# Optimization experiments

Measured on AMD Instinct MI355X. Metric: run time of the kernel, lower is better.

## Reference

```python
import jax, jax.numpy as jnp
import numpy as np

N_SRC0, N_DST0 = 100000, 20000   # block0: 100k src -> 20k dst
N_DST1 = 4096                    # block1: 20k src -> 4096 dst (seed nodes)


def setup_inputs() -> dict:
    key = jax.random.key(0)
    ks = jax.random.split(key, 8)
    E0, E1 = 640000, 131072
    return {
        "features": jax.random.normal(ks[0], (N_SRC0, 256), jnp.float32),
        "W1": jax.random.normal(ks[1], (256, 256), jnp.float32) * (1.0 / np.sqrt(256)),
        "b1": jnp.zeros((256,), jnp.float32),
        "W2": jax.random.normal(ks[2], (256, 128), jnp.float32) * (1.0 / np.sqrt(256)),
        "b2": jnp.zeros((128,), jnp.float32),
        "src0": jax.random.randint(ks[3], (E0,), 0, N_SRC0, jnp.int32),
        "dst0": jax.random.randint(ks[4], (E0,), 0, N_DST0, jnp.int32),
        "src1": jax.random.randint(ks[5], (E1,), 0, N_DST0, jnp.int32),
        "dst1": jax.random.randint(ks[6], (E1,), 0, N_DST1, jnp.int32),
    }


def _graph_conv(src, dst, n_dst, feat, W, b):
    # DGL GraphConv, norm='both': D_out^{-1/2} gather-sum D_in^{-1/2}, then WX+b.
    n_src = feat.shape[0]
    ones = jnp.ones(src.shape[0], feat.dtype)
    out_deg = jax.ops.segment_sum(ones, src, num_segments=n_src)
    norm_src = jnp.clip(out_deg, 1.0, None) ** -0.5          # [n_src]
    h = feat * norm_src[:, None]
    agg = jax.ops.segment_sum(h[src], dst, num_segments=n_dst)  # sparse SpMM
    in_deg = jax.ops.segment_sum(ones, dst, num_segments=n_dst)
    norm_dst = jnp.clip(in_deg, 1.0, None) ** -0.5           # [n_dst]
    return (agg * norm_dst[:, None]) @ W + b


def reference(features, W1, b1, W2, b2, src0, dst0, src1, dst1):
    x = jax.nn.relu(_graph_conv(src0, dst0, N_DST0, features, W1, b1))
    x = _graph_conv(src1, dst1, N_DST1, x, W2, b2)
    return x
```

## Files before the change

### kernel.cpp

```cpp
#include <hip/hip_runtime.h>
#include <hip/hip_bf16.h>

#define K_DIM 256
#define RSTRIDE 128

#define EPB   8192
#define G0_DB 625
#define G0_SB 256
#define G0_SW 392
#define G1_DB 128
#define G1_SB 64
#define G1_SW 313
#define BCAP  2048
#define SCAP  4096
#define GPAD  16

typedef short bf16x8 __attribute__((ext_vector_type(8)));
typedef float f32x4 __attribute__((ext_vector_type(4)));

static __device__ __forceinline__ unsigned short f2bf(float x) {
    __hip_bfloat16 b = __float2bfloat16(x);
    return *reinterpret_cast<unsigned short*>(&b);
}
static __device__ __forceinline__ float bflo(unsigned int p) {
    return __uint_as_float(p << 16);
}
static __device__ __forceinline__ float bfhi(unsigned int p) {
    return __uint_as_float(p & 0xffff0000u);
}

template <int NDB, int NSB, int SW>
static __device__ __forceinline__ void split_graph(
        const int* __restrict__ src, const int* __restrict__ dst, int E, int chunk,
        int* __restrict__ gdc, int* __restrict__ gsc,
        unsigned int* __restrict__ bdst, unsigned int* __restrict__ bsrc,
        int* sh) {
    int* histD = sh;
    int* histS = sh + NDB;
    int* baseD = sh + NDB + NSB;
    int* baseS = baseD + NDB;
    const int tid = threadIdx.x;
    const int e0 = chunk * EPB;
    const int n = min(EPB, E - e0);
    for (int i = tid; i < NDB + NSB; i += 256) sh[i] = 0;
    __syncthreads();
    for (int j = tid; j < n; j += 256) {
        int d = dst[e0 + j];
        int s = src[e0 + j];
        atomicAdd(&histD[d >> 5], 1);
        atomicAdd(&histS[(int)((unsigned)s / SW)], 1);
    }
    __syncthreads();
    for (int i = tid; i < NDB; i += 256) {
        int h = histD[i];
        baseD[i] = h ? atomicAdd(&gdc[i * GPAD], h) : 0;
        histD[i] = 0;
    }
    for (int i = tid; i < NSB; i += 256) {
        int h = histS[i];
        baseS[i] = h ? atomicAdd(&gsc[i * GPAD], h) : 0;
        histS[i] = 0;
    }
    __syncthreads();
    for (int j = tid; j < n; j += 256) {
        int d = dst[e0 + j];
        int s = src[e0 + j];
        int bD = d >> 5;
        int rD = atomicAdd(&histD[bD], 1) + baseD[bD];
        if (rD < BCAP) bdst[(size_t)bD * BCAP + rD] = ((unsigned)s << 5) | (unsigned)(d & 31);
        int bS = (int)((unsigned)s / SW);
        int rS = atomicAdd(&histS[bS], 1) + baseS[bS];
        if (rS < SCAP) bsrc[(size_t)bS * SCAP + rS] = (unsigned)s;
    }
}

__global__ __launch_bounds__(256) void split_mega_kernel(
        const int* __restrict__ src0, const int* __restrict__ dst0, int E0,
        const int* __restrict__ src1, const int* __restrict__ dst1, int E1,
        int* __restrict__ gdc0, int* __restrict__ gsc0,
        unsigned int* __restrict__ bdst0, unsigned int* __restrict__ bsrc0,
        int* __restrict__ gdc1, int* __restrict__ gsc1,
        unsigned int* __restrict__ bdst1, unsigned int* __restrict__ bsrc1,
        int nA0, int nA1,
        const float* __restrict__ feat, unsigned short* __restrict__ h, int total_f,
        int castBlocks,
        const float* __restrict__ W1, uint4* __restrict__ pw1,
        const float* __restrict__ W2, uint4* __restrict__ pw2) {
    __shared__ int sh[2 * (G0_DB + G0_SB)];
    const int b = blockIdx.x;
    if (b < nA0) {
        split_graph<G0_DB, G0_SB, G0_SW>(src0, dst0, E0, b, gdc0, gsc0, bdst0, bsrc0, sh);
    } else if (b < nA0 + nA1) {
        split_graph<G1_DB, G1_SB, G1_SW>(src1, dst1, E1, b - nA0, gdc1, gsc1, bdst1, bsrc1, sh);
    } else if (b < nA0 + nA1 + castBlocks) {
        int idx = ((b - nA0 - nA1) * blockDim.x + threadIdx.x) * 8;
        if (idx >= total_f) return;
        const float4 v0 = *reinterpret_cast<const float4*>(feat + idx);
        const float4 v1 = *reinterpret_cast<const float4*>(feat + idx + 4);
        union { ushort4 u4[2]; uint4 u; } o;
        o.u4[0].x = f2bf(v0.x); o.u4[0].y = f2bf(v0.y);
        o.u4[0].z = f2bf(v0.z); o.u4[0].w = f2bf(v0.w);
        o.u4[1].x = f2bf(v1.x); o.u4[1].y = f2bf(v1.y);
        o.u4[1].z = f2bf(v1.z); o.u4[1].w = f2bf(v1.w);
        *reinterpret_cast<uint4*>(h + idx) = o.u;
    } else if (b < nA0 + nA1 + castBlocks + 32) {
        int idx = (b - nA0 - nA1 - castBlocks) * blockDim.x + threadIdx.x;
        int lane = idx & 63;
        int kt = (idx >> 6) & 7;
        int nt = idx >> 9;
        int n = nt * 16 + (lane & 15);
        int k = kt * 32 + (lane >> 4) * 8;
        union { unsigned short us[8]; uint4 u; } o;
#pragma unroll
        for (int j = 0; j < 8; ++j) o.us[j] = f2bf(W1[(size_t)(k + j) * 256 + n]);
        pw1[idx] = o.u;
    } else {
        int idx = (b - nA0 - nA1 - castBlocks - 32) * blockDim.x + threadIdx.x;
        int lane = idx & 63;
        int kt = (idx >> 6) & 7;
        int nt = idx >> 9;
        int n = nt * 16 + (lane & 15);
        int k = kt * 32 + (lane >> 4) * 8;
        union { unsigned short us[8]; uint4 u; } o;
#pragma unroll
        for (int j = 0; j < 8; ++j) o.us[j] = f2bf(W2[(size_t)(k + j) * 128 + n]);
        pw2[idx] = o.u;
    }
}

__global__ __launch_bounds__(256) void finalize_kernel(
        const unsigned int* __restrict__ bdst0, const int* __restrict__ gdc0,
        int* __restrict__ cnt0, int* __restrict__ esrc0,
        const unsigned int* __restrict__ bdst1, const int* __restrict__ gdc1,
        int* __restrict__ cnt1, int* __restrict__ esrc1,
        const unsigned int* __restrict__ bsrc0, const int* __restrict__ gsc0,
        int* __restrict__ od0,
        const unsigned int* __restrict__ bsrc1, const int* __restrict__ gsc1,
        int* __restrict__ od1) {
    __shared__ int sh[G0_SW];
    const int tid = threadIdx.x;
    int b = blockIdx.x;
    if (b < G0_DB + G1_DB) {
        const bool g0 = b < G0_DB;
        if (!g0) b -= G0_DB;
        const unsigned int* __restrict__ bd = g0 ? bdst0 : bdst1;
        const int nb = min((g0 ? gdc0 : gdc1)[b * GPAD], BCAP);
        int* __restrict__ esrc = g0 ? esrc0 : esrc1;
        int* __restrict__ cnt = g0 ? cnt0 : cnt1;
        if (tid < 32) sh[tid] = 0;
        __syncthreads();
        for (int j = tid; j < nb; j += 256) {
            unsigned v = bd[(size_t)b * BCAP + j];
            int dloc = v & 31;
            int s = v >> 5;
            int slot = atomicAdd(&sh[dloc], 1);
            if (slot < RSTRIDE) esrc[((size_t)(b * 32 + dloc) << 7) + slot] = s;
        }
        __syncthreads();
        if (tid < 32) cnt[b * 32 + tid] = sh[tid];
    } else {
        b -= G0_DB + G1_DB;
        const bool g0 = b < G0_SB;
        if (!g0) b -= G0_SB;
        const unsigned int* __restrict__ bs = g0 ? bsrc0 : bsrc1;
        const int SW = g0 ? G0_SW : G1_SW;
        const int NN = g0 ? 100000 : 20000;
        const int nb = min((g0 ? gsc0 : gsc1)[b * GPAD], SCAP);
        int* __restrict__ od = g0 ? od0 : od1;
        for (int i = tid; i < SW; i += 256) sh[i] = 0;
        __syncthreads();
        const int base = b * SW;
        for (int j = tid; j < nb; j += 256) {
            int v = (int)bs[(size_t)b * SCAP + j];
            atomicAdd(&sh[v - base], 1);
        }
        __syncthreads();
        for (int i = tid; i < SW; i += 256) {
            int node = base + i;
            if (node < NN) od[node] = sh[i];
        }
    }
}

template <bool NORM>
__global__ __launch_bounds__(256) void gather_bf16_kernel(
        const unsigned short* __restrict__ hfeat, const int* __restrict__ esrc,
        const int* __restrict__ cnt, const int* __restrict__ od,
        unsigned short* __restrict__ aggb, int n_dst) {
    int row = blockIdx.x * (blockDim.x >> 6) + (threadIdx.x >> 6);
    int lane = threadIdx.x & 63;
    if (row >= n_dst) return;
    const int c = cnt[row];
    const int cend = min(c, RSTRIDE);
    const int* __restrict__ ep = esrc + ((size_t)row << 7);
    float a0 = 0.f, a1 = 0.f, a2 = 0.f, a3 = 0.f;
    int i = 0;
    for (; i + 3 < cend; i += 4) {
        int s0 = ep[i];
        int s1 = ep[i + 1];
        int s2 = ep[i + 2];
        int s3 = ep[i + 3];
        float n0 = NORM ? rsqrtf((float)max(od[s0], 1)) : 1.0f;
        float n1 = NORM ? rsqrtf((float)max(od[s1], 1)) : 1.0f;
        float n2 = NORM ? rsqrtf((float)max(od[s2], 1)) : 1.0f;
        float n3 = NORM ? rsqrtf((float)max(od[s3], 1)) : 1.0f;
        const uint2 p0 = *reinterpret_cast<const uint2*>(hfeat + (((size_t)s0) << 8) + lane * 4);
        const uint2 p1 = *reinterpret_cast<const uint2*>(hfeat + (((size_t)s1) << 8) + lane * 4);
        const uint2 p2 = *reinterpret_cast<const uint2*>(hfeat + (((size_t)s2) << 8) + lane * 4);
        const uint2 p3 = *reinterpret_cast<const uint2*>(hfeat + (((size_t)s3) << 8) + lane * 4);
        if (NORM) {
            a0 = fmaf(bflo(p0.x), n0, a0); a1 = fmaf(bfhi(p0.x), n0, a1);
            a2 = fmaf(bflo(p0.y), n0, a2); a3 = fmaf(bfhi(p0.y), n0, a3);
            a0 = fmaf(bflo(p1.x), n1, a0); a1 = fmaf(bfhi(p1.x), n1, a1);
            a2 = fmaf(bflo(p1.y), n1, a2); a3 = fmaf(bfhi(p1.y), n1, a3);
            a0 = fmaf(bflo(p2.x), n2, a0); a1 = fmaf(bfhi(p2.x), n2, a1);
            a2 = fmaf(bflo(p2.y), n2, a2); a3 = fmaf(bfhi(p2.y), n2, a3);
            a0 = fmaf(bflo(p3.x), n3, a0); a1 = fmaf(bfhi(p3.x), n3, a1);
            a2 = fmaf(bflo(p3.y), n3, a2); a3 = fmaf(bfhi(p3.y), n3, a3);
        } else {
            a0 += (bflo(p0.x) + bflo(p1.x)) + (bflo(p2.x) + bflo(p3.x));
            a1 += (bfhi(p0.x) + bfhi(p1.x)) + (bfhi(p2.x) + bfhi(p3.x));
            a2 += (bflo(p0.y) + bflo(p1.y)) + (bflo(p2.y) + bflo(p3.y));
            a3 += (bfhi(p0.y) + bfhi(p1.y)) + (bfhi(p2.y) + bfhi(p3.y));
        }
    }
    for (; i < cend; ++i) {
        int s0 = ep[i];
        float n0 = NORM ? rsqrtf((float)max(od[s0], 1)) : 1.0f;
        const uint2 p0 = *reinterpret_cast<const uint2*>(hfeat + (((size_t)s0) << 8) + lane * 4);
        if (NORM) {
            a0 = fmaf(bflo(p0.x), n0, a0); a1 = fmaf(bfhi(p0.x), n0, a1);
            a2 = fmaf(bflo(p0.y), n0, a2); a3 = fmaf(bfhi(p0.y), n0, a3);
        } else {
            a0 += bflo(p0.x);
            a1 += bfhi(p0.x);
            a2 += bflo(p0.y);
            a3 += bfhi(p0.y);
        }
    }
    float nd = rsqrtf((float)max(c, 1));
    ushort4 o;
    o.x = f2bf(a0 * nd);
    o.y = f2bf(a1 * nd);
    o.z = f2bf(a2 * nd);
    o.w = f2bf(a3 * nd);
    *reinterpret_cast<ushort4*>(aggb + (((size_t)row) << 8) + lane * 4) = o;
}

__global__ __launch_bounds__(256) void gemm0_mfma_kernel(
        const unsigned short* __restrict__ hA, const uint4* __restrict__ pW,
        const float* __restrict__ bias, const int* __restrict__ od1,
        unsigned short* __restrict__ out, int M) {
    const int m0 = blockIdx.x * 16;
    const int w = threadIdx.x >> 6;
    const int lane = threadIdx.x & 63;

    bf16x8 a[8];
    const unsigned short* ap = hA + (size_t)(m0 + (lane & 15)) * K_DIM + (lane >> 4) * 8;
#pragma unroll
    for (int kt = 0; kt < 8; ++kt)
        a[kt] = *reinterpret_cast<const bf16x8*>(ap + kt * 32);

    const int rbase = m0 + (lane >> 4) * 4;
    float nsv[4];
#pragma unroll
    for (int r = 0; r < 4; ++r) nsv[r] = rsqrtf((float)max(od1[rbase + r], 1));

#pragma unroll
    for (int nt = 0; nt < 4; ++nt) {
        const int n0 = w * 64 + nt * 16;
        f32x4 acc = {0.f, 0.f, 0.f, 0.f};
#pragma unroll
        for (int kt = 0; kt < 8; ++kt) {
            bf16x8 b = *reinterpret_cast<const bf16x8*>(&pW[((size_t)(n0 >> 4) * 8 + kt) * 64 + lane]);
            acc = __builtin_amdgcn_mfma_f32_16x16x32_bf16(a[kt], b, acc, 0, 0, 0);
        }
        const int col = n0 + (lane & 15);
        const float bv = bias[col];
#pragma unroll
        for (int r = 0; r < 4; ++r) {
            float v = fmaxf(acc[r] + bv, 0.0f) * nsv[r];
            out[(size_t)(rbase + r) * K_DIM + col] = f2bf(v);
        }
    }
}

__global__ __launch_bounds__(256) void gemm1_mfma_kernel(
        const unsigned short* __restrict__ hA, const uint4* __restrict__ pW,
        const float* __restrict__ bias, float* __restrict__ out, int M) {
    const int m0 = blockIdx.x * 16;
    const int w = threadIdx.x >> 6;
    const int lane = threadIdx.x & 63;

    bf16x8 a[8];
    const unsigned short* ap = hA + (size_t)(m0 + (lane & 15)) * K_DIM + (lane >> 4) * 8;
#pragma unroll
    for (int kt = 0; kt < 8; ++kt)
        a[kt] = *reinterpret_cast<const bf16x8*>(ap + kt * 32);

    const int rbase = m0 + (lane >> 4) * 4;
#pragma unroll
    for (int nt = 0; nt < 2; ++nt) {
        const int n0 = w * 32 + nt * 16;
        f32x4 acc = {0.f, 0.f, 0.f, 0.f};
#pragma unroll
        for (int kt = 0; kt < 8; ++kt) {
            bf16x8 b = *reinterpret_cast<const bf16x8*>(&pW[((size_t)(n0 >> 4) * 8 + kt) * 64 + lane]);
            acc = __builtin_amdgcn_mfma_f32_16x16x32_bf16(a[kt], b, acc, 0, 0, 0);
        }
        const int col = n0 + (lane & 15);
        const float bv = bias[col];
#pragma unroll
        for (int r = 0; r < 4; ++r)
            out[(size_t)(rbase + r) * 128 + col] = acc[r] + bv;
    }
}

__global__ __launch_bounds__(256) void gatherf_kernel(
        const float* __restrict__ feat, const int* __restrict__ esrc,
        const int* __restrict__ cnt, const int* __restrict__ od,
        float* __restrict__ outbuf, int n_dst) {
    int row = blockIdx.x * (blockDim.x >> 6) + (threadIdx.x >> 6);
    int lane = threadIdx.x & 63;
    if (row >= n_dst) return;
    const int c = cnt[row];
    const int cend = min(c, RSTRIDE);
    const int* __restrict__ ep = esrc + ((size_t)row << 7);
    float4 acc = {0.f, 0.f, 0.f, 0.f};
    for (int i = 0; i < cend; ++i) {
        int s0 = ep[i];
        float n0 = rsqrtf((float)max(od[s0], 1));
        const float4 v0 = *reinterpret_cast<const float4*>(feat + (((size_t)s0) << 8) + lane * 4);
        acc.x = fmaf(v0.x, n0, acc.x); acc.y = fmaf(v0.y, n0, acc.y);
        acc.z = fmaf(v0.z, n0, acc.z); acc.w = fmaf(v0.w, n0, acc.w);
    }
    float nd = rsqrtf((float)max(c, 1));
    float4 o = {acc.x * nd, acc.y * nd, acc.z * nd, acc.w * nd};
    *reinterpret_cast<float4*>(outbuf + (((size_t)row) << 8) + lane * 4) = o;
}

__global__ void edges_kernel(const int* __restrict__ src0, const int* __restrict__ dst0,
                             int* __restrict__ od0, int* __restrict__ cnt0,
                             int* __restrict__ esrc0, int E0,
                             const int* __restrict__ src1, const int* __restrict__ dst1,
                             int* __restrict__ od1, int* __restrict__ cnt1,
                             int* __restrict__ esrc1, int E1) {
    int i = blockIdx.x * blockDim.x + threadIdx.x;
    if (i < E0) {
        int s = src0[i];
        int d = dst0[i];
        atomicAdd(&od0[s], 1);
        int slot = atomicAdd(&cnt0[d], 1);
        if (slot < RSTRIDE) esrc0[(d << 7) + slot] = s;
    } else if (i < E0 + E1) {
        int e = i - E0;
        int s = src1[e];
        int d = dst1[e];
        atomicAdd(&od1[s], 1);
        int slot = atomicAdd(&cnt1[d], 1);
        if (slot < RSTRIDE) esrc1[(d << 7) + slot] = s;
    }
}

template <int ROWS, int NCOLS, bool RELU>
__global__ __launch_bounds__(NCOLS) void gemm_kernel(
        const float* __restrict__ A, const float* __restrict__ W,
        const float* __restrict__ bias, float* __restrict__ out, int M) {
    const int row0 = blockIdx.x * ROWS;
    const int c = threadIdx.x;
    const float* __restrict__ Ablk = A + (size_t)row0 * K_DIM;
    const float* __restrict__ Wc = W + c;

    float acc[ROWS];
#pragma unroll
    for (int r = 0; r < ROWS; ++r) acc[r] = 0.0f;

    float w0 = Wc[0];
    float w1 = Wc[NCOLS];
    float w2 = Wc[2 * NCOLS];
    float w3 = Wc[3 * NCOLS];

#pragma unroll 2
    for (int k = 0; k < K_DIM - 4; k += 4) {
        const float* p = Wc + (size_t)(k + 4) * NCOLS;
        float n0 = p[0];
        float n1 = p[NCOLS];
        float n2 = p[2 * NCOLS];
        float n3 = p[3 * NCOLS];
#pragma unroll
        for (int r = 0; r < ROWS; ++r) {
            const float4 a = *reinterpret_cast<const float4*>(Ablk + r * K_DIM + k);
            acc[r] = fmaf(a.x, w0, acc[r]);
            acc[r] = fmaf(a.y, w1, acc[r]);
            acc[r] = fmaf(a.z, w2, acc[r]);
            acc[r] = fmaf(a.w, w3, acc[r]);
        }
        w0 = n0; w1 = n1; w2 = n2; w3 = n3;
    }
    {
        const int k = K_DIM - 4;
#pragma unroll
        for (int r = 0; r < ROWS; ++r) {
            const float4 a = *reinterpret_cast<const float4*>(Ablk + r * K_DIM + k);
            acc[r] = fmaf(a.x, w0, acc[r]);
            acc[r] = fmaf(a.y, w1, acc[r]);
            acc[r] = fmaf(a.z, w2, acc[r]);
            acc[r] = fmaf(a.w, w3, acc[r]);
        }
    }

    const float b = bias[c];
#pragma unroll
    for (int r = 0; r < ROWS; ++r) {
        float v = acc[r] + b;
        if (RELU) v = fmaxf(v, 0.0f);
        out[(size_t)(row0 + r) * NCOLS + c] = v;
    }
}

extern "C" void kernel_launch(void* const* d_in, const int* in_sizes, int n_in,
                              void* d_out, int out_size, void* d_ws, size_t ws_size,
                              hipStream_t stream) {
    const float* features = (const float*)d_in[0];
    const float* W1 = (const float*)d_in[1];
    const float* b1 = (const float*)d_in[2];
    const float* W2 = (const float*)d_in[3];
    const float* b2 = (const float*)d_in[4];
    const int* src0 = (const int*)d_in[5];
    const int* dst0 = (const int*)d_in[6];
    const int* src1 = (const int*)d_in[7];
    const int* dst1 = (const int*)d_in[8];
    const int E0 = in_sizes[5];
    const int E1 = in_sizes[7];
    const int NSRC0 = 100000, NDST0 = 20000, NDST1 = 4096;

    char* ws = (char*)d_ws;
    size_t off = 0;
    auto carve = [&](size_t bytes) -> void* {
        void* p = ws + off;
        off = (off + bytes + 255) & ~(size_t)255;
        return p;
    };
    int* gdc0 = (int*)carve((size_t)G0_DB * GPAD * 4);
    int* gsc0 = (int*)carve((size_t)G0_SB * GPAD * 4);
    int* gdc1 = (int*)carve((size_t)G1_DB * GPAD * 4);
    int* gsc1 = (int*)carve((size_t)G1_SB * GPAD * 4);
    const size_t zero_span1 = off;
    int* od0  = (int*)carve((size_t)NSRC0 * 4);
    int* od1  = (int*)carve((size_t)NDST0 * 4);
    int* cnt0 = (int*)carve((size_t)NDST0 * 4);
    int* cnt1 = (int*)carve((size_t)NDST1 * 4);
    const size_t zero_span2 = off;
    uint4* pW1  = (uint4*)carve((size_t)8192 * 16);
    uint4* pW2  = (uint4*)carve((size_t)4096 * 16);
    unsigned int* bdst0 = (unsigned int*)carve((size_t)G0_DB * BCAP * 4);
    unsigned int* bsrc0 = (unsigned int*)carve((size_t)G0_SB * SCAP * 4);
    unsigned int* bdst1 = (unsigned int*)carve((size_t)G1_DB * BCAP * 4);
    unsigned int* bsrc1 = (unsigned int*)carve((size_t)G1_SB * SCAP * 4);
    int* esrc0p = (int*)carve((size_t)NDST0 * RSTRIDE * 4);
    int* esrc1p = (int*)carve((size_t)NDST1 * RSTRIDE * 4);
    unsigned short* aggb = (unsigned short*)carve((size_t)NDST0 * K_DIM * 2);
    const size_t hfeat_bytes = (size_t)NSRC0 * K_DIM * 2;
    const size_t xbufb_bytes = (size_t)NDST0 * K_DIM * 2;
    const size_t agg1b_bytes = (size_t)NDST1 * K_DIM * 2;
    const size_t need_bf16 = off + (hfeat_bytes > xbufb_bytes + agg1b_bytes
                                        ? hfeat_bytes : xbufb_bytes + agg1b_bytes);
    (void)n_in; (void)out_size;

    if (ws_size >= need_bf16) {
        unsigned short* hfeat = (unsigned short*)(ws + off);
        unsigned short* xbufb = (unsigned short*)(ws + off);
        unsigned short* agg1b = (unsigned short*)(ws + off + xbufb_bytes);

        hipMemsetAsync(ws, 0, zero_span1, stream);

        const int total_f = NSRC0 * K_DIM;
        const int nA0 = (E0 + EPB - 1) / EPB;
        const int nA1 = (E1 + EPB - 1) / EPB;
        const int castBlocks = (total_f / 8 + 255) / 256;
        split_mega_kernel<<<nA0 + nA1 + castBlocks + 48, 256, 0, stream>>>(
            src0, dst0, E0, src1, dst1, E1,
            gdc0, gsc0, bdst0, bsrc0, gdc1, gsc1, bdst1, bsrc1,
            nA0, nA1, features, hfeat, total_f, castBlocks,
            W1, pW1, W2, pW2);
        finalize_kernel<<<G0_DB + G1_DB + G0_SB + G1_SB, 256, 0, stream>>>(
            bdst0, gdc0, cnt0, esrc0p,
            bdst1, gdc1, cnt1, esrc1p,
            bsrc0, gsc0, od0,
            bsrc1, gsc1, od1);
        gather_bf16_kernel<true><<<(NDST0 + 3) / 4, 256, 0, stream>>>(
            hfeat, esrc0p, cnt0, od0, aggb, NDST0);
        gemm0_mfma_kernel<<<NDST0 / 16, 256, 0, stream>>>(aggb, pW1, b1, od1, xbufb, NDST0);
        gather_bf16_kernel<false><<<(NDST1 + 3) / 4, 256, 0, stream>>>(
            xbufb, esrc1p, cnt1, nullptr, agg1b, NDST1);
        gemm1_mfma_kernel<<<NDST1 / 16, 256, 0, stream>>>(agg1b, pW2, b2,
                                                          (float*)d_out, NDST1);
    } else {
        hipMemsetAsync(ws, 0, zero_span2, stream);
        float* agg0 = (float*)carve((size_t)NDST0 * K_DIM * 4);
        float* xbuf = (float*)carve((size_t)NDST0 * K_DIM * 4);
        float* agg1 = (float*)carve((size_t)NDST1 * K_DIM * 4);
        edges_kernel<<<(E0 + E1 + 255) / 256, 256, 0, stream>>>(
            src0, dst0, od0, cnt0, esrc0p, E0,
            src1, dst1, od1, cnt1, esrc1p, E1);
        gatherf_kernel<<<(NDST0 + 3) / 4, 256, 0, stream>>>(features, esrc0p, cnt0, od0,
                                                            agg0, NDST0);
        gemm_kernel<16, 256, true><<<NDST0 / 16, 256, 0, stream>>>(agg0, W1, b1, xbuf, NDST0);
        gatherf_kernel<<<(NDST1 + 3) / 4, 256, 0, stream>>>(xbuf, esrc1p, cnt1, od1,
                                                            agg1, NDST1);
        gemm_kernel<4, 128, false><<<NDST1 / 4, 128, 0, stream>>>(agg1, W2, b2,
                                                                  (float*)d_out, NDST1);
    }
}
```

Before: 283.1 us.

## Fuse gather into MFMA GEMMs and make edge bucketing single-pass per chunk

Edge bucketing now writes each chunk's edges into private per-chunk bucket segments in one pass. This removes the global atomic base reservation, the second pass over src/dst and the workspace memset. The finalize kernel walks the per-chunk segments for each bucket instead. Neighbour aggregation is fused into both MFMA GEMM kernels: each block gathers its 16 rows into LDS, dropping the bf16 aggregate round trip through global memory and two launches. The trade-offs are fewer concurrent waves available to hide gather latency, and small fixed per-chunk caps that could silently drop edges on skewed inputs.

```diff
diff --git a/kernel.cpp b/kernel.cpp
--- a/kernel.cpp
+++ b/kernel.cpp
@@ -3,17 +3,18 @@
 
 #define K_DIM 256
 #define RSTRIDE 128
-
-#define EPB   8192
+#define EPB 8192
+
 #define G0_DB 625
 #define G0_SB 256
 #define G0_SW 392
+#define G0_DCAP 48
+#define G0_SCAP 80
 #define G1_DB 128
 #define G1_SB 64
 #define G1_SW 313
-#define BCAP  2048
-#define SCAP  4096
-#define GPAD  16
+#define G1_DCAP 128
+#define G1_SCAP 224
 
 typedef short bf16x8 __attribute__((ext_vector_type(8)));
 typedef float f32x4 __attribute__((ext_vector_type(4)));
@@ -29,16 +30,12 @@
     return __uint_as_float(p & 0xffff0000u);
 }
 
-template <int NDB, int NSB, int SW>
-static __device__ __forceinline__ void split_graph(
+template <int NDB, int NSB, int SW, int DCAP, int SCP>
+static __device__ __forceinline__ void split_graph_sp(
         const int* __restrict__ src, const int* __restrict__ dst, int E, int chunk,
-        int* __restrict__ gdc, int* __restrict__ gsc,
+        int* __restrict__ gdcnt, int* __restrict__ gscnt,
         unsigned int* __restrict__ bdst, unsigned int* __restrict__ bsrc,
         int* sh) {
-    int* histD = sh;
-    int* histS = sh + NDB;
-    int* baseD = sh + NDB + NSB;
-    int* baseS = baseD + NDB;
     const int tid = threadIdx.x;
     const int e0 = chunk * EPB;
     const int n = min(EPB, E - e0);
@@ -47,51 +44,39 @@
     for (int j = tid; j < n; j += 256) {
         int d = dst[e0 + j];
         int s = src[e0 + j];
-        atomicAdd(&histD[d >> 5], 1);
-        atomicAdd(&histS[(int)((unsigned)s / SW)], 1);
+        int bD = d >> 5;
+        int rD = atomicAdd(&sh[bD], 1);
+        if (rD < DCAP) bdst[((size_t)chunk * NDB + bD) * DCAP + rD] =
+            ((unsigned)s << 5) | (unsigned)(d & 31);
+        int bS = (int)((unsigned)s / SW);
+        int rS = atomicAdd(&sh[NDB + bS], 1);
+        if (rS < SCP) bsrc[((size_t)chunk * NSB + bS) * SCP + rS] = (unsigned)s;
     }
     __syncthreads();
-    for (int i = tid; i < NDB; i += 256) {
-        int h = histD[i];
-        baseD[i] = h ? atomicAdd(&gdc[i * GPAD], h) : 0;
-        histD[i] = 0;
-    }
-    for (int i = tid; i < NSB; i += 256) {
-        int h = histS[i];
-        baseS[i] = h ? atomicAdd(&gsc[i * GPAD], h) : 0;
-        histS[i] = 0;
-    }
-    __syncthreads();
-    for (int j = tid; j < n; j += 256) {
-        int d = dst[e0 + j];
-        int s = src[e0 + j];
-        int bD = d >> 5;
-        int rD = atomicAdd(&histD[bD], 1) + baseD[bD];
-        if (rD < BCAP) bdst[(size_t)bD * BCAP + rD] = ((unsigned)s << 5) | (unsigned)(d & 31);
-        int bS = (int)((unsigned)s / SW);
-        int rS = atomicAdd(&histS[bS], 1) + baseS[bS];
-        if (rS < SCAP) bsrc[(size_t)bS * SCAP + rS] = (unsigned)s;
-    }
+    for (int i = tid; i < NDB; i += 256) gdcnt[chunk * NDB + i] = min(sh[i], DCAP);
+    for (int i = tid; i < NSB; i += 256) gscnt[chunk * NSB + i] = min(sh[NDB + i], SCP);
 }
 
 __global__ __launch_bounds__(256) void split_mega_kernel(
         const int* __restrict__ src0, const int* __restrict__ dst0, int E0,
         const int* __restrict__ src1, const int* __restrict__ dst1, int E1,
-        int* __restrict__ gdc0, int* __restrict__ gsc0,
+        int* __restrict__ gdcnt0, int* __restrict__ gscnt0,
         unsigned int* __restrict__ bdst0, unsigned int* __restrict__ bsrc0,
-        int* __restrict__ gdc1, int* __restrict__ gsc1,
+        int* __restrict__ gdcnt1, int* __restrict__ gscnt1,
         unsigned int* __restrict__ bdst1, unsigned int* __restrict__ bsrc1,
         int nA0, int nA1,
         const float* __restrict__ feat, unsigned short* __restrict__ h, int total_f,
         int castBlocks,
         const float* __restrict__ W1, uint4* __restrict__ pw1,
         const float* __restrict__ W2, uint4* __restrict__ pw2) {
-    __shared__ int sh[2 * (G0_DB + G0_SB)];
+    __shared__ int sh[G0_DB + G0_SB];
     const int b = blockIdx.x;
     if (b < nA0) {
-        split_graph<G0_DB, G0_SB, G0_SW>(src0, dst0, E0, b, gdc0, gsc0, bdst0, bsrc0, sh);
+        split_graph_sp<G0_DB, G0_SB, G0_SW, G0_DCAP, G0_SCAP>(
+            src0, dst0, E0, b, gdcnt0, gscnt0, bdst0, bsrc0, sh);
     } else if (b < nA0 + nA1) {
-        split_graph<G1_DB, G1_SB, G1_SW>(src1, dst1, E1, b - nA0, gdc1, gsc1, bdst1, bsrc1, sh);
+        split_graph_sp<G1_DB, G1_SB, G1_SW, G1_DCAP, G1_SCAP>(
+            src1, dst1, E1, b - nA0, gdcnt1, gscnt1, bdst1, bsrc1, sh);
     } else if (b < nA0 + nA1 + castBlocks) {
         int idx = ((b - nA0 - nA1) * blockDim.x + threadIdx.x) * 8;
         if (idx >= total_f) return;
@@ -129,13 +114,14 @@
 }
 
 __global__ __launch_bounds__(256) void finalize_kernel(
-        const unsigned int* __restrict__ bdst0, const int* __restrict__ gdc0,
+        int nA0, int nA1,
+        const unsigned int* __restrict__ bdst0, const int* __restrict__ gdcnt0,
         int* __restrict__ cnt0, int* __restrict__ esrc0,
-        const unsigned int* __restrict__ bdst1, const int* __restrict__ gdc1,
+        const unsigned int* __restrict__ bdst1, const int* __restrict__ gdcnt1,
         int* __restrict__ cnt1, int* __restrict__ esrc1,
-        const unsigned int* __restrict__ bsrc0, const int* __restrict__ gsc0,
+        const unsigned int* __restrict__ bsrc0, const int* __restrict__ gscnt0,
         int* __restrict__ od0,
-        const unsigned int* __restrict__ bsrc1, const int* __restrict__ gsc1,
+        const unsigned int* __restrict__ bsrc1, const int* __restrict__ gscnt1,
         int* __restrict__ od1) {
     __shared__ int sh[G0_SW];
     const int tid = threadIdx.x;
@@ -144,17 +130,24 @@
         const bool g0 = b < G0_DB;
         if (!g0) b -= G0_DB;
         const unsigned int* __restrict__ bd = g0 ? bdst0 : bdst1;
-        const int nb = min((g0 ? gdc0 : gdc1)[b * GPAD], BCAP);
+        const int* __restrict__ gc = g0 ? gdcnt0 : gdcnt1;
+        const int NDB = g0 ? G0_DB : G1_DB;
+        const int DCAP = g0 ? G0_DCAP : G1_DCAP;
+        const int nblk = g0 ? nA0 : nA1;
         int* __restrict__ esrc = g0 ? esrc0 : esrc1;
         int* __restrict__ cnt = g0 ? cnt0 : cnt1;
         if (tid < 32) sh[tid] = 0;
         __syncthreads();
-        for (int j = tid; j < nb; j += 256) {
-            unsigned v = bd[(size_t)b * BCAP + j];
-            int dloc = v & 31;
-            int s = v >> 5;
-            int slot = atomicAdd(&sh[dloc], 1);
-            if (slot < RSTRIDE) esrc[((size_t)(b * 32 + dloc) << 7) + slot] = s;
+        for (int rr = (tid >> 2); rr < nblk; rr += 64) {
+            const int c = gc[rr * NDB + b];
+            const unsigned int* __restrict__ seg = bd + ((size_t)rr * NDB + b) * DCAP;
+            for (int j = (tid & 3); j < c; j += 4) {
+                unsigned v = seg[j];
+                int dloc = v & 31;
+                int s = (int)(v >> 5);
+                int slot = atomicAdd(&sh[dloc], 1);
+                if (slot < RSTRIDE) esrc[((size_t)(b * 32 + dloc) << 7) + slot] = s;
+            }
         }
         __syncthreads();
         if (tid < 32) cnt[b * 32 + tid] = sh[tid];
@@ -163,16 +156,21 @@
         const bool g0 = b < G0_SB;
         if (!g0) b -= G0_SB;
         const unsigned int* __restrict__ bs = g0 ? bsrc0 : bsrc1;
+        const int* __restrict__ gc = g0 ? gscnt0 : gscnt1;
+        const int NSB = g0 ? G0_SB : G1_SB;
+        const int SCP = g0 ? G0_SCAP : G1_SCAP;
         const int SW = g0 ? G0_SW : G1_SW;
         const int NN = g0 ? 100000 : 20000;
-        const int nb = min((g0 ? gsc0 : gsc1)[b * GPAD], SCAP);
+        const int nblk = g0 ? nA0 : nA1;
         int* __restrict__ od = g0 ? od0 : od1;
         for (int i = tid; i < SW; i += 256) sh[i] = 0;
         __syncthreads();
         const int base = b * SW;
-        for (int j = tid; j < nb; j += 256) {
-            int v = (int)bs[(size_t)b * SCAP + j];
-            atomicAdd(&sh[v - base], 1);
+        for (int rr = (tid >> 2); rr < nblk; rr += 64) {
+            const int c = gc[rr * NSB + b];
+            const unsigned int* __restrict__ seg = bs + ((size_t)rr * NSB + b) * SCP;
+            for (int j = (tid & 3); j < c; j += 4)
+                atomicAdd(&sh[(int)seg[j] - base], 1);
         }
         __syncthreads();
         for (int i = tid; i < SW; i += 256) {
@@ -183,80 +181,86 @@
 }
 
 template <bool NORM>
-__global__ __launch_bounds__(256) void gather_bf16_kernel(
+static __device__ __forceinline__ void gather4_to_lds(
         const unsigned short* __restrict__ hfeat, const int* __restrict__ esrc,
         const int* __restrict__ cnt, const int* __restrict__ od,
-        unsigned short* __restrict__ aggb, int n_dst) {
-    int row = blockIdx.x * (blockDim.x >> 6) + (threadIdx.x >> 6);
-    int lane = threadIdx.x & 63;
-    if (row >= n_dst) return;
-    const int c = cnt[row];
-    const int cend = min(c, RSTRIDE);
-    const int* __restrict__ ep = esrc + ((size_t)row << 7);
-    float a0 = 0.f, a1 = 0.f, a2 = 0.f, a3 = 0.f;
-    int i = 0;
-    for (; i + 3 < cend; i += 4) {
-        int s0 = ep[i];
-        int s1 = ep[i + 1];
-        int s2 = ep[i + 2];
-        int s3 = ep[i + 3];
-        float n0 = NORM ? rsqrtf((float)max(od[s0], 1)) : 1.0f;
-        float n1 = NORM ? rsqrtf((float)max(od[s1], 1)) : 1.0f;
-        float n2 = NORM ? rsqrtf((float)max(od[s2], 1)) : 1.0f;
-        float n3 = NORM ? rsqrtf((float)max(od[s3], 1)) : 1.0f;
-        const uint2 p0 = *reinterpret_cast<const uint2*>(hfeat + (((size_t)s0) << 8) + lane * 4);
-        const uint2 p1 = *reinterpret_cast<const uint2*>(hfeat + (((size_t)s1) << 8) + lane * 4);
-        const uint2 p2 = *reinterpret_cast<const uint2*>(hfeat + (((size_t)s2) << 8) + lane * 4);
-        const uint2 p3 = *reinterpret_cast<const uint2*>(hfeat + (((size_t)s3) << 8) + lane * 4);
-        if (NORM) {
-            a0 = fmaf(bflo(p0.x), n0, a0); a1 = fmaf(bfhi(p0.x), n0, a1);
-            a2 = fmaf(bflo(p0.y), n0, a2); a3 = fmaf(bfhi(p0.y), n0, a3);
-            a0 = fmaf(bflo(p1.x), n1, a0); a1 = fmaf(bfhi(p1.x), n1, a1);
-            a2 = fmaf(bflo(p1.y), n1, a2); a3 = fmaf(bfhi(p1.y), n1, a3);
-            a0 = fmaf(bflo(p2.x), n2, a0); a1 = fmaf(bfhi(p2.x), n2, a1);
-            a2 = fmaf(bflo(p2.y), n2, a2); a3 = fmaf(bfhi(p2.y), n2, a3);
-            a0 = fmaf(bflo(p3.x), n3, a0); a1 = fmaf(bfhi(p3.x), n3, a1);
-            a2 = fmaf(bflo(p3.y), n3, a2); a3 = fmaf(bfhi(p3.y), n3, a3);
-        } else {
-            a0 += (bflo(p0.x) + bflo(p1.x)) + (bflo(p2.x) + bflo(p3.x));
-            a1 += (bfhi(p0.x) + bfhi(p1.x)) + (bfhi(p2.x) + bfhi(p3.x));
-            a2 += (bflo(p0.y) + bflo(p1.y)) + (bflo(p2.y) + bflo(p3.y));
-            a3 += (bfhi(p0.y) + bfhi(p1.y)) + (bfhi(p2.y) + bfhi(p3.y));
-        }
-    }
-    for (; i < cend; ++i) {
-        int s0 = ep[i];
-        float n0 = NORM ? rsqrtf((float)max(od[s0], 1)) : 1.0f;
-        const uint2 p0 = *reinterpret_cast<const uint2*>(hfeat + (((size_t)s0) << 8) + lane * 4);
-        if (NORM) {
-            a0 = fmaf(bflo(p0.x), n0, a0); a1 = fmaf(bfhi(p0.x), n0, a1);
-            a2 = fmaf(bflo(p0.y), n0, a2); a3 = fmaf(bfhi(p0.y), n0, a3);
-        } else {
-            a0 += bflo(p0.x);
-            a1 += bfhi(p0.x);
-            a2 += bflo(p0.y);
-            a3 += bfhi(p0.y);
-        }
-    }
-    float nd = rsqrtf((float)max(c, 1));
-    ushort4 o;
-    o.x = f2bf(a0 * nd);
-    o.y = f2bf(a1 * nd);
-    o.z = f2bf(a2 * nd);
-    o.w = f2bf(a3 * nd);
-    *reinterpret_cast<ushort4*>(aggb + (((size_t)row) << 8) + lane * 4) = o;
-}
-
-__global__ __launch_bounds__(256) void gemm0_mfma_kernel(
-        const unsigned short* __restrict__ hA, const uint4* __restrict__ pW,
-        const float* __restrict__ bias, const int* __restrict__ od1,
-        unsigned short* __restrict__ out, int M) {
+        int m0, int w, int lane, unsigned short (*Alds)[264]) {
+#pragma unroll
+    for (int k = 0; k < 4; ++k) {
+        const int rloc = w * 4 + k;
+        const int row = m0 + rloc;
+        const int c = cnt[row];
+        const int cend = min(c, RSTRIDE);
+        const int* __restrict__ ep = esrc + ((size_t)row << 7);
+        float a0 = 0.f, a1 = 0.f, a2 = 0.f, a3 = 0.f;
+        int i = 0;
+        for (; i + 3 < cend; i += 4) {
+            int s0 = ep[i];
+            int s1 = ep[i + 1];
+            int s2 = ep[i + 2];
+            int s3 = ep[i + 3];
+            float n0 = NORM ? rsqrtf((float)max(od[s0], 1)) : 1.0f;
+            float n1 = NORM ? rsqrtf((float)max(od[s1], 1)) : 1.0f;
+            float n2 = NORM ? rsqrtf((float)max(od[s2], 1)) : 1.0f;
+            float n3 = NORM ? rsqrtf((float)max(od[s3], 1)) : 1.0f;
+            const uint2 p0 = *reinterpret_cast<const uint2*>(hfeat + (((size_t)s0) << 8) + lane * 4);
+            const uint2 p1 = *reinterpret_cast<const uint2*>(hfeat + (((size_t)s1) << 8) + lane * 4);
+            const uint2 p2 = *reinterpret_cast<const uint2*>(hfeat + (((size_t)s2) << 8) + lane * 4);
+            const uint2 p3 = *reinterpret_cast<const uint2*>(hfeat + (((size_t)s3) << 8) + lane * 4);
+            if (NORM) {
+                a0 = fmaf(bflo(p0.x), n0, a0); a1 = fmaf(bfhi(p0.x), n0, a1);
+                a2 = fmaf(bflo(p0.y), n0, a2); a3 = fmaf(bfhi(p0.y), n0, a3);
+                a0 = fmaf(bflo(p1.x), n1, a0); a1 = fmaf(bfhi(p1.x), n1, a1);
+                a2 = fmaf(bflo(p1.y), n1, a2); a3 = fmaf(bfhi(p1.y), n1, a3);
+                a0 = fmaf(bflo(p2.x), n2, a0); a1 = fmaf(bfhi(p2.x), n2, a1);
+                a2 = fmaf(bflo(p2.y), n2, a2); a3 = fmaf(bfhi(p2.y), n2, a3);
+                a0 = fmaf(bflo(p3.x), n3, a0); a1 = fmaf(bfhi(p3.x), n3, a1);
+                a2 = fmaf(bflo(p3.y), n3, a2); a3 = fmaf(bfhi(p3.y), n3, a3);
+            } else {
+                a0 += (bflo(p0.x) + bflo(p1.x)) + (bflo(p2.x) + bflo(p3.x));
+                a1 += (bfhi(p0.x) + bfhi(p1.x)) + (bfhi(p2.x) + bfhi(p3.x));
+                a2 += (bflo(p0.y) + bflo(p1.y)) + (bflo(p2.y) + bflo(p3.y));
+                a3 += (bfhi(p0.y) + bfhi(p1.y)) + (bfhi(p2.y) + bfhi(p3.y));
+            }
+        }
+        for (; i < cend; ++i) {
+            int s0 = ep[i];
+            float n0 = NORM ? rsqrtf((float)max(od[s0], 1)) : 1.0f;
+            const uint2 p0 = *reinterpret_cast<const uint2*>(hfeat + (((size_t)s0) << 8) + lane * 4);
+            if (NORM) {
+                a0 = fmaf(bflo(p0.x), n0, a0); a1 = fmaf(bfhi(p0.x), n0, a1);
+                a2 = fmaf(bflo(p0.y), n0, a2); a3 = fmaf(bfhi(p0.y), n0, a3);
+            } else {
+                a0 += bflo(p0.x);
+                a1 += bfhi(p0.x);
+                a2 += bflo(p0.y);
+                a3 += bfhi(p0.y);
+            }
+        }
+        float nd = rsqrtf((float)max(c, 1));
+        ushort4 o;
+        o.x = f2bf(a0 * nd);
+        o.y = f2bf(a1 * nd);
+        o.z = f2bf(a2 * nd);
+        o.w = f2bf(a3 * nd);
+        *reinterpret_cast<ushort4*>(&Alds[rloc][lane * 4]) = o;
+    }
+}
+
+__global__ __launch_bounds__(256) void fused0_kernel(
+        const unsigned short* __restrict__ hfeat, const int* __restrict__ esrc,
+        const int* __restrict__ cnt, const int* __restrict__ od0,
+        const uint4* __restrict__ pW, const float* __restrict__ bias,
+        const int* __restrict__ od1, unsigned short* __restrict__ out) {
+    __shared__ unsigned short Alds[16][264];
     const int m0 = blockIdx.x * 16;
     const int w = threadIdx.x >> 6;
     const int lane = threadIdx.x & 63;
+    gather4_to_lds<true>(hfeat, esrc, cnt, od0, m0, w, lane, Alds);
+    __syncthreads();
 
     bf16x8 a[8];
-    const unsigned short* ap = hA + (size_t)(m0 + (lane & 15)) * K_DIM + (lane >> 4) * 8;
+    const unsigned short* ap = &Alds[lane & 15][(lane >> 4) * 8];
 #pragma unroll
     for (int kt = 0; kt < 8; ++kt)
         a[kt] = *reinterpret_cast<const bf16x8*>(ap + kt * 32);
@@ -285,15 +289,20 @@
     }
 }
 
-__global__ __launch_bounds__(256) void gemm1_mfma_kernel(
-        const unsigned short* __restrict__ hA, const uint4* __restrict__ pW,
-        const float* __restrict__ bias, float* __restrict__ out, int M) {
+__global__ __launch_bounds__(256) void fused1_kernel(
+        const unsigned short* __restrict__ xb, const int* __restrict__ esrc,
+        const int* __restrict__ cnt,
+        const uint4* __restrict__ pW, const float* __restrict__ bias,
+        float* __restrict__ out) {
+    __shared__ unsigned short Alds[16][264];
     const int m0 = blockIdx.x * 16;
     const int w = threadIdx.x >> 6;
     const int lane = threadIdx.x & 63;
+    gather4_to_lds<false>(xb, esrc, cnt, nullptr, m0, w, lane, Alds);
+    __syncthreads();
 
     bf16x8 a[8];
-    const unsigned short* ap = hA + (size_t)(m0 + (lane & 15)) * K_DIM + (lane >> 4) * 8;
+    const unsigned short* ap = &Alds[lane & 15][(lane >> 4) * 8];
 #pragma unroll
     for (int kt = 0; kt < 8; ++kt)
         a[kt] = *reinterpret_cast<const bf16x8*>(ap + kt * 32);
@@ -433,6 +442,8 @@
     const int E0 = in_sizes[5];
     const int E1 = in_sizes[7];
     const int NSRC0 = 100000, NDST0 = 20000, NDST1 = 4096;
+    const int nA0 = (E0 + EPB - 1) / EPB;
+    const int nA1 = (E1 + EPB - 1) / EPB;
 
     char* ws = (char*)d_ws;
     size_t off = 0;
@@ -441,62 +452,54 @@
         off = (off + bytes + 255) & ~(size_t)255;
         return p;
     };
-    int* gdc0 = (int*)carve((size_t)G0_DB * GPAD * 4);
-    int* gsc0 = (int*)carve((size_t)G0_SB * GPAD * 4);
-    int* gdc1 = (int*)carve((size_t)G1_DB * GPAD * 4);
-    int* gsc1 = (int*)carve((size_t)G1_SB * GPAD * 4);
-    const size_t zero_span1 = off;
     int* od0  = (int*)carve((size_t)NSRC0 * 4);
     int* od1  = (int*)carve((size_t)NDST0 * 4);
     int* cnt0 = (int*)carve((size_t)NDST0 * 4);
     int* cnt1 = (int*)carve((size_t)NDST1 * 4);
-    const size_t zero_span2 = off;
+    const size_t zero_span = off;
+    int* esrc0p = (int*)carve((size_t)NDST0 * RSTRIDE * 4);
+    int* esrc1p = (int*)carve((size_t)NDST1 * RSTRIDE * 4);
     uint4* pW1  = (uint4*)carve((size_t)8192 * 16);
     uint4* pW2  = (uint4*)carve((size_t)4096 * 16);
-    unsigned int* bdst0 = (unsigned int*)carve((size_t)G0_DB * BCAP * 4);
-    unsigned int* bsrc0 = (unsigned int*)carve((size_t)G0_SB * SCAP * 4);
-    unsigned int* bdst1 = (unsigned int*)carve((size_t)G1_DB * BCAP * 4);
-    unsigned int* bsrc1 = (unsigned int*)carve((size_t)G1_SB * SCAP * 4);
-    int* esrc0p = (int*)carve((size_t)NDST0 * RSTRIDE * 4);
-    int* esrc1p = (int*)carve((size_t)NDST1 * RSTRIDE * 4);
-    unsigned short* aggb = (unsigned short*)carve((size_t)NDST0 * K_DIM * 2);
+    int* gdcnt0 = (int*)carve((size_t)nA0 * G0_DB * 4);
+    int* gscnt0 = (int*)carve((size_t)nA0 * G0_SB * 4);
+    int* gdcnt1 = (int*)carve((size_t)nA1 * G1_DB * 4);
+    int* gscnt1 = (int*)carve((size_t)nA1 * G1_SB * 4);
+    unsigned int* bdst0 = (unsigned int*)carve((size_t)nA0 * G0_DB * G0_DCAP * 4);
+    unsigned int* bsrc0 = (unsigned int*)carve((size_t)nA0 * G0_SB * G0_SCAP * 4);
+    unsigned int* bdst1 = (unsigned int*)carve((size_t)nA1 * G1_DB * G1_DCAP * 4);
+    unsigned int* bsrc1 = (unsigned int*)carve((size_t)nA1 * G1_SB * G1_SCAP * 4);
+    const size_t region_span = (size_t)((ws + off) - (char*)bdst0);
+    const size_t xbufb_bytes = (size_t)NDST0 * K_DIM * 2;
+    unsigned short* xbufb = (region_span >= xbufb_bytes)
+        ? (unsigned short*)bdst0
+        : (unsigned short*)carve(xbufb_bytes);
     const size_t hfeat_bytes = (size_t)NSRC0 * K_DIM * 2;
-    const size_t xbufb_bytes = (size_t)NDST0 * K_DIM * 2;
-    const size_t agg1b_bytes = (size_t)NDST1 * K_DIM * 2;
-    const size_t need_bf16 = off + (hfeat_bytes > xbufb_bytes + agg1b_bytes
-                                        ? hfeat_bytes : xbufb_bytes + agg1b_bytes);
+    unsigned short* hfeat = (unsigned short*)carve(hfeat_bytes);
+    const size_t need_bf16 = off;
     (void)n_in; (void)out_size;
 
     if (ws_size >= need_bf16) {
-        unsigned short* hfeat = (unsigned short*)(ws + off);
-        unsigned short* xbufb = (unsigned short*)(ws + off);
-        unsigned short* agg1b = (unsigned short*)(ws + off + xbufb_bytes);
-
-        hipMemsetAsync(ws, 0, zero_span1, stream);
-
         const int total_f = NSRC0 * K_DIM;
-        const int nA0 = (E0 + EPB - 1) / EPB;
-        const int nA1 = (E1 + EPB - 1) / EPB;
         const int castBlocks = (total_f / 8 + 255) / 256;
         split_mega_kernel<<<nA0 + nA1 + castBlocks + 48, 256, 0, stream>>>(
             src0, dst0, E0, src1, dst1, E1,
-            gdc0, gsc0, bdst0, bsrc0, gdc1, gsc1, bdst1, bsrc1,
+            gdcnt0, gscnt0, bdst0, bsrc0,
+            gdcnt1, gscnt1, bdst1, bsrc1,
             nA0, nA1, features, hfeat, total_f, castBlocks,
             W1, pW1, W2, pW2);
         finalize_kernel<<<G0_DB + G1_DB + G0_SB + G1_SB, 256, 0, stream>>>(
-            bdst0, gdc0, cnt0, esrc0p,
-            bdst1, gdc1, cnt1, esrc1p,
-            bsrc0, gsc0, od0,
-            bsrc1, gsc1, od1);
-        gather_bf16_kernel<true><<<(NDST0 + 3) / 4, 256, 0, stream>>>(
-            hfeat, esrc0p, cnt0, od0, aggb, NDST0);
-        gemm0_mfma_kernel<<<NDST0 / 16, 256, 0, stream>>>(aggb, pW1, b1, od1, xbufb, NDST0);
-        gather_bf16_kernel<false><<<(NDST1 + 3) / 4, 256, 0, stream>>>(
-            xbufb, esrc1p, cnt1, nullptr, agg1b, NDST1);
-        gemm1_mfma_kernel<<<NDST1 / 16, 256, 0, stream>>>(agg1b, pW2, b2,
-                                                          (float*)d_out, NDST1);
+            nA0, nA1,
+            bdst0, gdcnt0, cnt0, esrc0p,
+            bdst1, gdcnt1, cnt1, esrc1p,
+            bsrc0, gscnt0, od0,
+            bsrc1, gscnt1, od1);
+        fused0_kernel<<<NDST0 / 16, 256, 0, stream>>>(
+            hfeat, esrc0p, cnt0, od0, pW1, b1, od1, xbufb);
+        fused1_kernel<<<NDST1 / 16, 256, 0, stream>>>(
+            xbufb, esrc1p, cnt1, pW2, b2, (float*)d_out);
     } else {
-        hipMemsetAsync(ws, 0, zero_span2, stream);
+        hipMemsetAsync(ws, 0, zero_span, stream);
         float* agg0 = (float*)carve((size_t)NDST0 * K_DIM * 4);
         float* xbuf = (float*)carve((size_t)NDST0 * K_DIM * 4);
         float* agg1 = (float*)carve((size_t)NDST1 * K_DIM * 4);
```

Measured after the change: 318.2 us. +12.4%, slower.
